# Performance work log

Hardware: AMD Instinct MI355X
Metric: run time of the kernel (lower is better)

The kernel has to match this reference:

```python
import jax, jax.numpy as jnp
import numpy as np

K = 512
HIDDEN = 256


def setup_inputs() -> dict:
    key = jax.random.key(0)
    k1, k2 = jax.random.split(key)
    z = jax.random.normal(k1, (8, 8192, HIDDEN), dtype=jnp.float32)
    # codebook init: uniform(-1/k, 1/k) as in the torch module
    codebook = jax.random.uniform(k2, (K, HIDDEN), dtype=jnp.float32,
                                  minval=-1.0 / K, maxval=1.0 / K)
    return {"z": z, "codebook": codebook}


def reference(z, codebook):
    # squared L2 distance to every code, expanded form to avoid the
    # [N, k, hidden] intermediate: ||z||^2 - 2 z.c + ||c||^2
    z2 = jnp.sum(z * z, axis=-1, keepdims=True)            # [B, T, 1]
    c2 = jnp.sum(codebook * codebook, axis=-1)             # [k]
    cross = jnp.einsum('bth,kh->btk', z, codebook)         # [B, T, k]
    distances = z2 - 2.0 * cross + c2                      # [B, T, k]
    ind = jnp.argmin(distances, axis=-1)                   # [B, T] int
    z_q = codebook[ind]                                    # [B, T, hidden]

    vq_loss = jnp.mean((z_q - jax.lax.stop_gradient(z)) ** 2)
    commitment_loss = jnp.mean((z - jax.lax.stop_gradient(z_q)) ** 2)
    z_q_st = z + jax.lax.stop_gradient(z_q - z)
    return (z_q_st, ind, vq_loss + commitment_loss)
```

## Files before the change

### kernel.cpp

```cpp
#include <hip/hip_runtime.h>

#define M_TOKENS 65536
#define HID      256
#define KCODES   512

#define IND_OFF  (M_TOKENS * HID)
#define LOSS_OFF (IND_OFF + M_TOKENS)

#define TAU      1.5e-4f

#define WS_C2_OFF        16
#define WS_BHI_OFF       4096
#define WS_BLO_OFF       (4096 + 262144)
#define WS_LIST_OFF_FAST (4096 + 524288)
#define WS_LIST_OFF_SLOW 4096
#define WS_MIN_FAST      (WS_LIST_OFF_FAST + 8192 * 4)

typedef __attribute__((ext_vector_type(8))) short  short8;
typedef __attribute__((ext_vector_type(4))) float  f32x4;

__device__ inline unsigned short f2bf(float f) {
    unsigned u = __float_as_uint(f);
    u += 0x7FFF + ((u >> 16) & 1);
    return (unsigned short)(u >> 16);
}
__device__ inline float bf2f(unsigned short h) {
    return __uint_as_float(((unsigned)h) << 16);
}

__global__ __launch_bounds__(256) void vq_prep(
    const float* __restrict__ cb,
    unsigned short* __restrict__ Bhi, unsigned short* __restrict__ Blo,
    float* __restrict__ c2, double* __restrict__ acc, int* __restrict__ cnt) {
    int b = blockIdx.x;
    if (b < 64) {
        int g = b * 256 + threadIdx.x;
        int frag = g >> 6, lane = g & 63;
        int nb = frag >> 3, kb = frag & 7;
        int code = nb * 16 + (lane & 15);
        int kk = kb * 32 + (lane >> 4) * 8;
        const float4* s4 = reinterpret_cast<const float4*>(cb + code * HID + kk);
        float4 v0 = s4[0], v1 = s4[1];
        float f[8] = {v0.x, v0.y, v0.z, v0.w, v1.x, v1.y, v1.z, v1.w};
        short8 vh, vl;
        #pragma unroll
        for (int j = 0; j < 8; ++j) {
            unsigned short h = f2bf(f[j]);
            vh[j] = (short)h;
            vl[j] = (short)f2bf(f[j] - bf2f(h));
        }
        *reinterpret_cast<short8*>(Bhi + (size_t)g * 8) = vh;
        *reinterpret_cast<short8*>(Blo + (size_t)g * 8) = vl;
    } else {
        if (b == 64 && threadIdx.x == 0) { *acc = 0.0; *cnt = 0; }
        int k = (b - 64) * 256 + threadIdx.x;
        const float* row = cb + k * HID;
        double s = 0.0;
        for (int i = 0; i < HID; ++i) {
            double v = (double)row[i];
            s = fma(v, v, s);
        }
        c2[k] = (float)s;
    }
}

__global__ __launch_bounds__(256, 2) void vq_main_mfma(
    const float* __restrict__ z, const float* __restrict__ cb,
    const float* __restrict__ c2g,
    const unsigned short* __restrict__ Bhi,
    const unsigned short* __restrict__ Blo,
    float* __restrict__ out, double* __restrict__ loss_acc,
    int* __restrict__ cnt, int* __restrict__ list, int cap) {

    __shared__ short8 ldsB[2][32][64];
    __shared__ float  lds_c2[KCODES];

    const int tid  = threadIdx.x;
    const int wid  = tid >> 6;
    const int lane = tid & 63;
    const int q    = lane >> 4;
    const int tokW = blockIdx.x * 128 + wid * 32;

    const float4* z4  = reinterpret_cast<const float4*>(z);
    const float4* cb4 = reinterpret_cast<const float4*>(cb);

    lds_c2[tid]       = c2g[tid];
    lds_c2[tid + 256] = c2g[tid + 256];

#define STAGE(kv, bufv) do {                                                   \
        _Pragma("unroll")                                                      \
        for (int j = 0; j < 8; ++j) {                                          \
            int s_  = (wid << 3) | j;                                          \
            int g_  = s_ >> 4;                                                 \
            int t_  = s_ & 15;                                                 \
            int kb_ = t_ & 7;                                                  \
            const unsigned short* src_ =                                       \
                ((t_ < 8) ? Bhi : Blo) +                                       \
                (((size_t)((2 * (kv) + g_) * 8 + kb_) * 64 + lane) << 3);      \
            __builtin_amdgcn_global_load_lds(                                  \
                (const __attribute__((address_space(1))) void*)src_,           \
                (__attribute__((address_space(3))) void*)&ldsB[bufv][s_][0],   \
                16, 0, 0);                                                     \
        }                                                                      \
    } while (0)

    STAGE(0, 0);

    short8 ah[2][8], al[2][8];
    float sq[2];
    #pragma unroll
    for (int mf = 0; mf < 2; ++mf) {
        int token = tokW + mf * 16 + (lane & 15);
        const float4* zr = z4 + (size_t)token * 64 + q * 2;
        float s = 0.f;
        #pragma unroll
        for (int kb = 0; kb < 8; ++kb) {
            float4 v0 = zr[kb * 8];
            float4 v1 = zr[kb * 8 + 1];
            float f[8] = {v0.x, v0.y, v0.z, v0.w, v1.x, v1.y, v1.z, v1.w};
            short8 vh, vl;
            #pragma unroll
            for (int j = 0; j < 8; ++j) {
                unsigned short h = f2bf(f[j]);
                vh[j] = (short)h;
                vl[j] = (short)f2bf(f[j] - bf2f(h));
                s = fmaf(f[j], f[j], s);
            }
            ah[mf][kb] = vh;
            al[mf][kb] = vl;
        }
        s += __shfl_xor(s, 16, 64);
        s += __shfl_xor(s, 32, 64);
        sq[mf] = s;
    }

    float b1[2][4], b2[2][4];
    int   i1[2][4];
    #pragma unroll
    for (int mf = 0; mf < 2; ++mf)
        #pragma unroll
        for (int r = 0; r < 4; ++r) { b1[mf][r] = 3.4e38f; b2[mf][r] = 3.4e38f; i1[mf][r] = 0; }

    #pragma unroll 2
    for (int k = 0; k < 16; ++k) {
        int buf = k & 1;
        __syncthreads();
        if (k < 15) STAGE(k + 1, buf ^ 1);

        #pragma unroll
        for (int g = 0; g < 2; ++g) {
            f32x4 a0 = {0.f, 0.f, 0.f, 0.f};
            f32x4 a1 = {0.f, 0.f, 0.f, 0.f};
            __builtin_amdgcn_s_setprio(1);
            #pragma unroll
            for (int kb = 0; kb < 8; ++kb) {
                short8 vbh = ldsB[buf][g * 16 + kb][lane];
                short8 vbl = ldsB[buf][g * 16 + 8 + kb][lane];
                a0 = __builtin_amdgcn_mfma_f32_16x16x32_bf16(ah[0][kb], vbh, a0, 0, 0, 0);
                a1 = __builtin_amdgcn_mfma_f32_16x16x32_bf16(ah[1][kb], vbh, a1, 0, 0, 0);
                a0 = __builtin_amdgcn_mfma_f32_16x16x32_bf16(al[0][kb], vbh, a0, 0, 0, 0);
                a1 = __builtin_amdgcn_mfma_f32_16x16x32_bf16(al[1][kb], vbh, a1, 0, 0, 0);
                a0 = __builtin_amdgcn_mfma_f32_16x16x32_bf16(ah[0][kb], vbl, a0, 0, 0, 0);
                a1 = __builtin_amdgcn_mfma_f32_16x16x32_bf16(ah[1][kb], vbl, a1, 0, 0, 0);
            }
            __builtin_amdgcn_s_setprio(0);
            int code = (2 * k + g) * 16 + (lane & 15);
            float c2v = lds_c2[code];
            #pragma unroll
            for (int r = 0; r < 4; ++r) {
                float s0 = fmaf(-2.f, a0[r], c2v);
                if (s0 < b1[0][r]) { b2[0][r] = b1[0][r]; b1[0][r] = s0; i1[0][r] = code; }
                else if (s0 < b2[0][r]) b2[0][r] = s0;
                float s1 = fmaf(-2.f, a1[r], c2v);
                if (s1 < b1[1][r]) { b2[1][r] = b1[1][r]; b1[1][r] = s1; i1[1][r] = code; }
                else if (s1 < b2[1][r]) b2[1][r] = s1;
            }
        }
    }
#undef STAGE

    #pragma unroll
    for (int st = 1; st <= 8; st <<= 1) {
        #pragma unroll
        for (int mf = 0; mf < 2; ++mf)
            #pragma unroll
            for (int r = 0; r < 4; ++r) {
                float ob1 = __shfl_xor(b1[mf][r], st, 64);
                int   oi1 = __shfl_xor(i1[mf][r], st, 64);
                float ob2 = __shfl_xor(b2[mf][r], st, 64);
                if (ob1 < b1[mf][r] || (ob1 == b1[mf][r] && oi1 < i1[mf][r])) {
                    b2[mf][r] = fminf(b1[mf][r], ob2);
                    b1[mf][r] = ob1;
                    i1[mf][r] = oi1;
                } else {
                    b2[mf][r] = fminf(b2[mf][r], ob1);
                }
            }
    }

    if ((lane & 15) == 0) {
        #pragma unroll
        for (int mf = 0; mf < 2; ++mf) {
            float4 iv;
            #pragma unroll
            for (int r = 0; r < 4; ++r) {
                ((float*)&iv)[r] = (float)i1[mf][r];
                if (b2[mf][r] - b1[mf][r] <= TAU) {
                    int pos = atomicAdd(cnt, 1);
                    if (pos < cap) list[pos] = tokW + mf * 16 + q * 4 + r;
                }
            }
            *reinterpret_cast<float4*>(out + IND_OFF + tokW + mf * 16 + q * 4) = iv;
        }
    }

    double lsum = 0.0;
    #pragma unroll
    for (int mf = 0; mf < 2; ++mf)
        #pragma unroll
        for (int r = 0; r < 4; ++r) {
            float z2r = __shfl(sq[mf], (lane & 48) | (q * 4 + r), 64);
            if ((lane & 15) == 0) lsum += (double)z2r + (double)b1[mf][r];
        }
    lsum += __shfl_xor(lsum, 16, 64);
    lsum += __shfl_xor(lsum, 32, 64);
    if (lane == 0) atomicAdd(loss_acc, lsum);

    float4* out4 = reinterpret_cast<float4*>(out);
    #pragma unroll
    for (int tt = 0; tt < 32; ++tt) {
        int code = __shfl(i1[tt >> 4][tt & 3], ((tt >> 2) & 3) * 16, 64);
        float4 cv = cb4[(size_t)code * 64 + lane];
        out4[(size_t)(tokW + tt) * 64 + lane] = cv;
    }
}

#define BM   128
#define NC   128
#define KS   32
#define PAD  33

__global__ void vq_init(const float* __restrict__ cb, float* __restrict__ c2,
                        double* __restrict__ acc, int* __restrict__ cnt) {
    int k = threadIdx.x;
    if (k == 0) { *acc = 0.0; *cnt = 0; }
    const float* row = cb + k * HID;
    double s = 0.0;
    for (int i = 0; i < HID; ++i) {
        double v = (double)row[i];
        s = fma(v, v, s);
    }
    c2[k] = (float)s;
}

__global__ __launch_bounds__(256, 2) void vq_main_f32(
    const float* __restrict__ z, const float* __restrict__ cb,
    const float* __restrict__ c2g, float* __restrict__ out,
    double* __restrict__ loss_acc, int* __restrict__ cnt,
    int* __restrict__ list, int cap) {

    __shared__ float smem[(BM + NC) * PAD];
    float* zs = smem;
    float* cs = smem + BM * PAD;

    const int tid = threadIdx.x;
    const int tx = tid & 15;
    const int ty = tid >> 4;
    const int tokBase = blockIdx.x * BM;

    const float4* z4g  = reinterpret_cast<const float4*>(z);
    const float4* cb4g = reinterpret_cast<const float4*>(cb);

    float bs[8], bs2[8];
    int   bi[8];
    #pragma unroll
    for (int m = 0; m < 8; ++m) { bs[m] = 3.4e38f; bs2[m] = 3.4e38f; bi[m] = 0; }

    for (int chunk = 0; chunk < KCODES / NC; ++chunk) {
        float acc[8][8];
        #pragma unroll
        for (int m = 0; m < 8; ++m)
            #pragma unroll
            for (int n = 0; n < 8; ++n) acc[m][n] = 0.f;

        for (int ks = 0; ks < HID / KS; ++ks) {
            __syncthreads();
            #pragma unroll
            for (int i = 0; i < 4; ++i) {
                int f   = tid + i * 256;
                int row = f >> 3;
                int k4  = f & 7;
                float4 zv = z4g[(tokBase + row) * (HID / 4) + ks * (KS / 4) + k4];
                int b = row * PAD + k4 * 4;
                zs[b + 0] = zv.x; zs[b + 1] = zv.y; zs[b + 2] = zv.z; zs[b + 3] = zv.w;
                float4 cv = cb4g[(chunk * NC + row) * (HID / 4) + ks * (KS / 4) + k4];
                cs[b + 0] = cv.x; cs[b + 1] = cv.y; cs[b + 2] = cv.z; cs[b + 3] = cv.w;
            }
            __syncthreads();

            #pragma unroll 2
            for (int k = 0; k < KS; ++k) {
                float zf[8], cf[8];
                #pragma unroll
                for (int m = 0; m < 8; ++m) zf[m] = zs[(ty * 8 + m) * PAD + k];
                #pragma unroll
                for (int n = 0; n < 8; ++n) cf[n] = cs[(tx * 8 + n) * PAD + k];
                #pragma unroll
                for (int m = 0; m < 8; ++m)
                    #pragma unroll
                    for (int n = 0; n < 8; ++n)
                        acc[m][n] = fmaf(zf[m], cf[n], acc[m][n]);
            }
        }

        #pragma unroll
        for (int n = 0; n < 8; ++n) {
            int code = chunk * NC + tx * 8 + n;
            float c2v = c2g[code];
            #pragma unroll
            for (int m = 0; m < 8; ++m) {
                float s = fmaf(-2.f, acc[m][n], c2v);
                if (s < bs[m]) { bs2[m] = bs[m]; bs[m] = s; bi[m] = code; }
                else if (s < bs2[m]) bs2[m] = s;
            }
        }
    }

    __syncthreads();
    float* rs   = smem;
    int*   ri   = reinterpret_cast<int*>(smem + BM * 16);
    float* rs2  = smem + BM * 32;
    int*   inds = reinterpret_cast<int*>(smem + BM * 48);
    float* wred = smem + BM * 48 + BM;

    #pragma unroll
    for (int m = 0; m < 8; ++m) {
        int tok = ty * 8 + m;
        rs [tok * 16 + tx] = bs[m];
        ri [tok * 16 + tx] = bi[m];
        rs2[tok * 16 + tx] = bs2[m];
    }
    __syncthreads();

    if (tid < BM) {
        float B1 = rs[tid * 16];
        int   I1 = ri[tid * 16];
        float B2 = rs2[tid * 16];
        for (int j = 1; j < 16; ++j) {
            float b1v = rs [tid * 16 + j];
            int   i1v = ri [tid * 16 + j];
            float b2v = rs2[tid * 16 + j];
            if (b1v < B1 || (b1v == B1 && i1v < I1)) {
                B2 = fminf(B1, b2v); B1 = b1v; I1 = i1v;
            } else {
                B2 = fminf(B2, b1v);
            }
        }
        inds[tid] = I1;
        out[IND_OFF + tokBase + tid] = (float)I1;
        if (B2 - B1 <= TAU) {
            int pos = atomicAdd(cnt, 1);
            if (pos < cap) list[pos] = tokBase + tid;
        }
    }
    __syncthreads();

    float loc = 0.f;
    float4* out4 = reinterpret_cast<float4*>(out);
    for (int it = 0; it < (BM * HID / 4) / 256; ++it) {
        int e4  = it * 256 + tid;
        int tok = e4 >> 6;
        int h4  = e4 & 63;
        int code = inds[tok];
        float4 cv = cb4g[code * 64 + h4];
        float4 zv = z4g[(tokBase + tok) * 64 + h4];
        out4[(tokBase + tok) * 64 + h4] = cv;
        float dx = cv.x - zv.x, dy = cv.y - zv.y;
        float dz = cv.z - zv.z, dw = cv.w - zv.w;
        loc = fmaf(dx, dx, loc);
        loc = fmaf(dy, dy, loc);
        loc = fmaf(dz, dz, loc);
        loc = fmaf(dw, dw, loc);
    }
    #pragma unroll
    for (int off = 32; off > 0; off >>= 1) loc += __shfl_xor(loc, off, 64);
    int wave = tid >> 6;
    if ((tid & 63) == 0) wred[wave] = loc;
    __syncthreads();
    if (tid == 0) {
        double t = (double)wred[0] + (double)wred[1] +
                   (double)wred[2] + (double)wred[3];
        atomicAdd(loss_acc, t);
    }
}

#define RT 8
__global__ __launch_bounds__(256) void vq_refine(
    const float* __restrict__ z, const float* __restrict__ cb,
    const float* __restrict__ c2g, const double* __restrict__ loss_acc,
    const int* __restrict__ cnt, const int* __restrict__ list,
    float* __restrict__ out, int cap) {

    if (blockIdx.x == 0 && threadIdx.x == 0)
        out[LOSS_OFF] = (float)(2.0 * (*loss_acc) / (double)(M_TOKENS * HID));

    __shared__ float  zrow[RT][HID];
    __shared__ double redd[RT][256];
    __shared__ int    redi[RT][256];

    const int tid = threadIdx.x;
    int n = *cnt; if (n > cap) n = cap;

    for (int base = blockIdx.x * RT; base < n; base += gridDim.x * RT) {
        int toks[RT];
        #pragma unroll
        for (int t = 0; t < RT; ++t) {
            int ii = base + t;
            if (ii > n - 1) ii = n - 1;
            toks[t] = list[ii];
        }
        #pragma unroll
        for (int t = 0; t < RT; ++t) {
            float v = z[(size_t)toks[t] * HID + tid];
            zrow[t][tid] = v;
            redd[t][tid] = (double)v * (double)v;
        }
        __syncthreads();
        for (int s = 128; s > 0; s >>= 1) {
            if (tid < s) {
                #pragma unroll
                for (int t = 0; t < RT; ++t) redd[t][tid] += redd[t][tid + s];
            }
            __syncthreads();
        }
        float z2f[RT];
        #pragma unroll
        for (int t = 0; t < RT; ++t) z2f[t] = (float)redd[t][0];
        __syncthreads();

        double bd[RT];
        int    bk[RT];
        #pragma unroll
        for (int t = 0; t < RT; ++t) { bd[t] = 1e300; bk[t] = 1 << 30; }

        for (int c = 0; c < 2; ++c) {
            int k = tid + c * 256;
            const float4* cr = reinterpret_cast<const float4*>(cb + (size_t)k * HID);
            double acc[RT];
            #pragma unroll
            for (int t = 0; t < RT; ++t) acc[t] = 0.0;
            for (int i = 0; i < HID / 4; ++i) {
                float4 cv = cr[i];
                #pragma unroll
                for (int t = 0; t < RT; ++t) {
                    float4 zv = *reinterpret_cast<const float4*>(&zrow[t][i * 4]);
                    acc[t] = fma((double)zv.x, (double)cv.x, acc[t]);
                    acc[t] = fma((double)zv.y, (double)cv.y, acc[t]);
                    acc[t] = fma((double)zv.z, (double)cv.z, acc[t]);
                    acc[t] = fma((double)zv.w, (double)cv.w, acc[t]);
                }
            }
            float c2v = c2g[k];
            #pragma unroll
            for (int t = 0; t < RT; ++t) {
                float cross32 = (float)acc[t];
                float u = 2.0f * cross32;
                float tq = (float)((double)z2f[t] - (double)u);
                float D = (float)((double)tq + (double)c2v);
                double Dd = (double)D;
                if (Dd < bd[t] || (Dd == bd[t] && k < bk[t])) { bd[t] = Dd; bk[t] = k; }
            }
        }
        #pragma unroll
        for (int t = 0; t < RT; ++t) { redd[t][tid] = bd[t]; redi[t][tid] = bk[t]; }
        __syncthreads();
        for (int s = 128; s > 0; s >>= 1) {
            if (tid < s) {
                #pragma unroll
                for (int t = 0; t < RT; ++t) {
                    double d2 = redd[t][tid + s]; int i2v = redi[t][tid + s];
                    if (d2 < redd[t][tid] ||
                        (d2 == redd[t][tid] && i2v < redi[t][tid])) {
                        redd[t][tid] = d2; redi[t][tid] = i2v;
                    }
                }
            }
            __syncthreads();
        }
        if (tid < RT) out[IND_OFF + toks[tid]] = (float)redi[tid][0];
        #pragma unroll
        for (int t = 0; t < RT; ++t) {
            int best = redi[t][0];
            out[(size_t)toks[t] * HID + tid] = cb[(size_t)best * HID + tid];
        }
        __syncthreads();
    }
}

extern "C" void kernel_launch(void* const* d_in, const int* in_sizes, int n_in,
                              void* d_out, int out_size, void* d_ws, size_t ws_size,
                              hipStream_t stream) {
    const float* z  = (const float*)d_in[0];
    const float* cb = (const float*)d_in[1];
    float* out = (float*)d_out;
    double* acc = (double*)d_ws;
    int*  cnt = (int*)((char*)d_ws + 8);
    float* c2 = (float*)((char*)d_ws + WS_C2_OFF);

    if (ws_size >= WS_MIN_FAST) {
        unsigned short* Bhi = (unsigned short*)((char*)d_ws + WS_BHI_OFF);
        unsigned short* Blo = (unsigned short*)((char*)d_ws + WS_BLO_OFF);
        int* list = (int*)((char*)d_ws + WS_LIST_OFF_FAST);
        int cap = 8192;
        vq_prep<<<66, 256, 0, stream>>>(cb, Bhi, Blo, c2, acc, cnt);
        vq_main_mfma<<<M_TOKENS / 128, 256, 0, stream>>>(
            z, cb, c2, Bhi, Blo, out, acc, cnt, list, cap);
        vq_refine<<<128, 256, 0, stream>>>(z, cb, c2, acc, cnt, list, out, cap);
    } else {
        int* list = (int*)((char*)d_ws + WS_LIST_OFF_SLOW);
        int cap = 0;
        if (ws_size > WS_LIST_OFF_SLOW + 16) {
            size_t avail = (ws_size - WS_LIST_OFF_SLOW) / 4;
            cap = (avail > 8192) ? 8192 : (int)avail;
        }
        vq_init<<<1, 512, 0, stream>>>(cb, c2, acc, cnt);
        vq_main_f32<<<M_TOKENS / BM, 256, 0, stream>>>(
            z, cb, c2, out, acc, cnt, list, cap);
        vq_refine<<<128, 256, 0, stream>>>(z, cb, c2, acc, cnt, list, out, cap);
    }
}
```

Before: 177.7 us.

## Replace split-bf16 triple MFMA with single scaled fp16 MFMA and wider refine

```diff
diff --git a/kernel.cpp b/kernel.cpp
--- a/kernel.cpp
+++ b/kernel.cpp
@@ -7,30 +7,20 @@
 #define IND_OFF  (M_TOKENS * HID)
 #define LOSS_OFF (IND_OFF + M_TOKENS)
 
-#define TAU      1.5e-4f
+#define TAU      3e-4f
 
 #define WS_C2_OFF        16
 #define WS_BHI_OFF       4096
-#define WS_BLO_OFF       (4096 + 262144)
-#define WS_LIST_OFF_FAST (4096 + 524288)
+#define WS_LIST_OFF_FAST (4096 + 262144)
 #define WS_LIST_OFF_SLOW 4096
-#define WS_MIN_FAST      (WS_LIST_OFF_FAST + 8192 * 4)
-
-typedef __attribute__((ext_vector_type(8))) short  short8;
-typedef __attribute__((ext_vector_type(4))) float  f32x4;
-
-__device__ inline unsigned short f2bf(float f) {
-    unsigned u = __float_as_uint(f);
-    u += 0x7FFF + ((u >> 16) & 1);
-    return (unsigned short)(u >> 16);
-}
-__device__ inline float bf2f(unsigned short h) {
-    return __uint_as_float(((unsigned)h) << 16);
-}
+#define WS_MIN_FAST      (WS_LIST_OFF_FAST + 65536 * 4)
+
+typedef __attribute__((ext_vector_type(8))) _Float16 f16x8;
+typedef __attribute__((ext_vector_type(4))) float    f32x4;
 
 __global__ __launch_bounds__(256) void vq_prep(
     const float* __restrict__ cb,
-    unsigned short* __restrict__ Bhi, unsigned short* __restrict__ Blo,
+    unsigned short* __restrict__ Bhi,
     float* __restrict__ c2, double* __restrict__ acc, int* __restrict__ cnt) {
     int b = blockIdx.x;
     if (b < 64) {
@@ -42,15 +32,11 @@
         const float4* s4 = reinterpret_cast<const float4*>(cb + code * HID + kk);
         float4 v0 = s4[0], v1 = s4[1];
         float f[8] = {v0.x, v0.y, v0.z, v0.w, v1.x, v1.y, v1.z, v1.w};
-        short8 vh, vl;
-        #pragma unroll
-        for (int j = 0; j < 8; ++j) {
-            unsigned short h = f2bf(f[j]);
-            vh[j] = (short)h;
-            vl[j] = (short)f2bf(f[j] - bf2f(h));
-        }
-        *reinterpret_cast<short8*>(Bhi + (size_t)g * 8) = vh;
-        *reinterpret_cast<short8*>(Blo + (size_t)g * 8) = vl;
+        f16x8 vh;
+        #pragma unroll
+        for (int j = 0; j < 8; ++j)
+            vh[j] = (_Float16)(f[j] * 512.0f);
+        *reinterpret_cast<f16x8*>(Bhi + (size_t)g * 8) = vh;
     } else {
         if (b == 64 && threadIdx.x == 0) { *acc = 0.0; *cnt = 0; }
         int k = (b - 64) * 256 + threadIdx.x;
@@ -68,12 +54,11 @@
     const float* __restrict__ z, const float* __restrict__ cb,
     const float* __restrict__ c2g,
     const unsigned short* __restrict__ Bhi,
-    const unsigned short* __restrict__ Blo,
     float* __restrict__ out, double* __restrict__ loss_acc,
     int* __restrict__ cnt, int* __restrict__ list, int cap) {
 
-    __shared__ short8 ldsB[2][32][64];
-    __shared__ float  lds_c2[KCODES];
+    __shared__ f16x8 ldsB[2][32][64];
+    __shared__ float lds_c2[KCODES];
 
     const int tid  = threadIdx.x;
     const int wid  = tid >> 6;
@@ -90,23 +75,19 @@
 #define STAGE(kv, bufv) do {                                                   \
         _Pragma("unroll")                                                      \
         for (int j = 0; j < 8; ++j) {                                          \
-            int s_  = (wid << 3) | j;                                          \
-            int g_  = s_ >> 4;                                                 \
-            int t_  = s_ & 15;                                                 \
-            int kb_ = t_ & 7;                                                  \
-            const unsigned short* src_ =                                       \
-                ((t_ < 8) ? Bhi : Blo) +                                       \
-                (((size_t)((2 * (kv) + g_) * 8 + kb_) * 64 + lane) << 3);      \
+            const unsigned short* src_ = Bhi +                                 \
+                (((size_t)((4 * (kv) + wid) * 8 + j) * 64 + lane) << 3);       \
             __builtin_amdgcn_global_load_lds(                                  \
                 (const __attribute__((address_space(1))) void*)src_,           \
-                (__attribute__((address_space(3))) void*)&ldsB[bufv][s_][0],   \
+                (__attribute__((address_space(3))) void*)                      \
+                    &ldsB[bufv][(wid << 3) | j][0],                            \
                 16, 0, 0);                                                     \
         }                                                                      \
     } while (0)
 
     STAGE(0, 0);
 
-    short8 ah[2][8], al[2][8];
+    f16x8 ah[2][8];
     float sq[2];
     #pragma unroll
     for (int mf = 0; mf < 2; ++mf) {
@@ -118,16 +99,13 @@
             float4 v0 = zr[kb * 8];
             float4 v1 = zr[kb * 8 + 1];
             float f[8] = {v0.x, v0.y, v0.z, v0.w, v1.x, v1.y, v1.z, v1.w};
-            short8 vh, vl;
+            f16x8 vh;
             #pragma unroll
             for (int j = 0; j < 8; ++j) {
-                unsigned short h = f2bf(f[j]);
-                vh[j] = (short)h;
-                vl[j] = (short)f2bf(f[j] - bf2f(h));
+                vh[j] = (_Float16)f[j];
                 s = fmaf(f[j], f[j], s);
             }
             ah[mf][kb] = vh;
-            al[mf][kb] = vl;
         }
         s += __shfl_xor(s, 16, 64);
         s += __shfl_xor(s, 32, 64);
@@ -142,36 +120,31 @@
         for (int r = 0; r < 4; ++r) { b1[mf][r] = 3.4e38f; b2[mf][r] = 3.4e38f; i1[mf][r] = 0; }
 
     #pragma unroll 2
-    for (int k = 0; k < 16; ++k) {
+    for (int k = 0; k < 8; ++k) {
         int buf = k & 1;
         __syncthreads();
-        if (k < 15) STAGE(k + 1, buf ^ 1);
-
-        #pragma unroll
-        for (int g = 0; g < 2; ++g) {
+        if (k < 7) STAGE(k + 1, buf ^ 1);
+
+        #pragma unroll
+        for (int g = 0; g < 4; ++g) {
             f32x4 a0 = {0.f, 0.f, 0.f, 0.f};
             f32x4 a1 = {0.f, 0.f, 0.f, 0.f};
             __builtin_amdgcn_s_setprio(1);
             #pragma unroll
             for (int kb = 0; kb < 8; ++kb) {
-                short8 vbh = ldsB[buf][g * 16 + kb][lane];
-                short8 vbl = ldsB[buf][g * 16 + 8 + kb][lane];
-                a0 = __builtin_amdgcn_mfma_f32_16x16x32_bf16(ah[0][kb], vbh, a0, 0, 0, 0);
-                a1 = __builtin_amdgcn_mfma_f32_16x16x32_bf16(ah[1][kb], vbh, a1, 0, 0, 0);
-                a0 = __builtin_amdgcn_mfma_f32_16x16x32_bf16(al[0][kb], vbh, a0, 0, 0, 0);
-                a1 = __builtin_amdgcn_mfma_f32_16x16x32_bf16(al[1][kb], vbh, a1, 0, 0, 0);
-                a0 = __builtin_amdgcn_mfma_f32_16x16x32_bf16(ah[0][kb], vbl, a0, 0, 0, 0);
-                a1 = __builtin_amdgcn_mfma_f32_16x16x32_bf16(ah[1][kb], vbl, a1, 0, 0, 0);
+                f16x8 vb = ldsB[buf][g * 8 + kb][lane];
+                a0 = __builtin_amdgcn_mfma_f32_16x16x32_f16(ah[0][kb], vb, a0, 0, 0, 0);
+                a1 = __builtin_amdgcn_mfma_f32_16x16x32_f16(ah[1][kb], vb, a1, 0, 0, 0);
             }
             __builtin_amdgcn_s_setprio(0);
-            int code = (2 * k + g) * 16 + (lane & 15);
+            int code = (4 * k + g) * 16 + (lane & 15);
             float c2v = lds_c2[code];
             #pragma unroll
             for (int r = 0; r < 4; ++r) {
-                float s0 = fmaf(-2.f, a0[r], c2v);
+                float s0 = fmaf(-0.00390625f, a0[r], c2v);
                 if (s0 < b1[0][r]) { b2[0][r] = b1[0][r]; b1[0][r] = s0; i1[0][r] = code; }
                 else if (s0 < b2[0][r]) b2[0][r] = s0;
-                float s1 = fmaf(-2.f, a1[r], c2v);
+                float s1 = fmaf(-0.00390625f, a1[r], c2v);
                 if (s1 < b1[1][r]) { b2[1][r] = b1[1][r]; b1[1][r] = s1; i1[1][r] = code; }
                 else if (s1 < b2[1][r]) b2[1][r] = s1;
             }
@@ -509,13 +482,12 @@
 
     if (ws_size >= WS_MIN_FAST) {
         unsigned short* Bhi = (unsigned short*)((char*)d_ws + WS_BHI_OFF);
-        unsigned short* Blo = (unsigned short*)((char*)d_ws + WS_BLO_OFF);
         int* list = (int*)((char*)d_ws + WS_LIST_OFF_FAST);
-        int cap = 8192;
-        vq_prep<<<66, 256, 0, stream>>>(cb, Bhi, Blo, c2, acc, cnt);
+        int cap = 65536;
+        vq_prep<<<66, 256, 0, stream>>>(cb, Bhi, c2, acc, cnt);
         vq_main_mfma<<<M_TOKENS / 128, 256, 0, stream>>>(
-            z, cb, c2, Bhi, Blo, out, acc, cnt, list, cap);
-        vq_refine<<<128, 256, 0, stream>>>(z, cb, c2, acc, cnt, list, out, cap);
+            z, cb, c2, Bhi, out, acc, cnt, list, cap);
+        vq_refine<<<192, 256, 0, stream>>>(z, cb, c2, acc, cnt, list, out, cap);
     } else {
         int* list = (int*)((char*)d_ws + WS_LIST_OFF_SLOW);
         int cap = 0;
@@ -526,6 +498,6 @@
         vq_init<<<1, 512, 0, stream>>>(cb, c2, acc, cnt);
         vq_main_f32<<<M_TOKENS / BM, 256, 0, stream>>>(
             z, cb, c2, out, acc, cnt, list, cap);
-        vq_refine<<<128, 256, 0, stream>>>(z, cb, c2, acc, cnt, list, out, cap);
+        vq_refine<<<192, 256, 0, stream>>>(z, cb, c2, acc, cnt, list, out, cap);
     }
 }
```

New measurement: 229.6 us. 29.2% more time.
